# Optimization experiments

Measured on AMD Instinct MI355X. Metric: run time of the kernel, lower is better.

Reference implementation:

```python
import jax, jax.numpy as jnp
import numpy as np

N, E, F_IN, NCLS, H = 50000, 800000, 128, 10, 64


def setup_inputs() -> dict:
    key = jax.random.key(0)
    ks = jax.random.split(key, 24)
    p = lambda k, shp: (jax.random.normal(k, shp, dtype=jnp.float32) * 0.1)
    inp = {
        'x': jax.random.normal(ks[0], (N, F_IN), dtype=jnp.float32),
        'edge_index': jax.random.randint(ks[1], (2, E), 0, N, dtype=jnp.int64),
        'gcn1_W': p(ks[2], (F_IN, 128)), 'gcn1_b': p(ks[3], (128,)),
        'gcn2_W': p(ks[4], (128, 64)),  'gcn2_b': p(ks[5], (64,)),
        'gcn3_W': p(ks[6], (64, 32)),   'gcn3_b': p(ks[7], (32,)),
        'gat_W': p(ks[8], (32, 32)), 'gat_a_src': p(ks[9], (32,)),
        'gat_a_dst': p(ks[10], (32,)), 'gat_b': p(ks[11], (32,)),
        'lstm_Wih_f': p(ks[12], (4 * H, 32)), 'lstm_bih_f': p(ks[13], (4 * H,)), 'lstm_bhh_f': p(ks[14], (4 * H,)),
        'lstm_Wih_b': p(ks[15], (4 * H, 32)), 'lstm_bih_b': p(ks[16], (4 * H,)), 'lstm_bhh_b': p(ks[17], (4 * H,)),
        'bn_gamma': jnp.ones((2 * H,), jnp.float32), 'bn_beta': jnp.zeros((2 * H,), jnp.float32),
        'fc_W': p(ks[18], (NCLS, 2 * H)), 'fc_b': p(ks[19], (NCLS,)),
    }
    return inp


def _forward(x, edge_index, gcn1_W, gcn1_b, gcn2_W, gcn2_b, gcn3_W, gcn3_b,
             gat_W, gat_a_src, gat_a_dst, gat_b,
             lstm_Wih_f, lstm_bih_f, lstm_bhh_f, lstm_Wih_b, lstm_bih_b, lstm_bhh_b,
             bn_gamma, bn_beta, fc_W, fc_b):
    n = x.shape[0]
    loop = jnp.arange(n)
    row = jnp.concatenate([edge_index[0], loop])  # source nodes (+ self loops)
    col = jnp.concatenate([edge_index[1], loop])  # target nodes
    deg = jax.ops.segment_sum(jnp.ones_like(col, dtype=x.dtype), col, num_segments=n)
    dis = jax.lax.rsqrt(jnp.maximum(deg, 1e-12))  # deg >= 1 due to self loops
    norm = dis[row] * dis[col]

    def gcn(h, W, b):
        h = h @ W
        return jax.ops.segment_sum(h[row] * norm[:, None], col, num_segments=n) + b

    h = jax.nn.relu(gcn(x, gcn1_W, gcn1_b))
    h = jax.nn.relu(gcn(h, gcn2_W, gcn2_b))
    h = gcn(h, gcn3_W, gcn3_b)

    # GAT (1 head), self loops already in row/col, softmax over incoming edges per target
    g = h @ gat_W
    e = jax.nn.leaky_relu((g @ gat_a_src)[row] + (g @ gat_a_dst)[col], negative_slope=0.2)
    m = jax.ops.segment_max(e, col, num_segments=n)
    ee = jnp.exp(e - m[col])
    att = ee / jax.ops.segment_sum(ee, col, num_segments=n)[col]
    h = jax.ops.segment_sum(g[row] * att[:, None], col, num_segments=n) + gat_b
    h = jax.nn.relu(h)

    # bidirectional LSTM with seq_len=1, h0=c0=0 -> single cell step per direction
    def lstm_dir(xx, Wih, bih, bhh):
        gt = xx @ Wih.T + bih + bhh
        i, f, c, o = jnp.split(gt, 4, axis=-1)  # torch gate order i,f,g,o
        return jax.nn.sigmoid(o) * jnp.tanh(jax.nn.sigmoid(i) * jnp.tanh(c))

    r = jnp.concatenate([lstm_dir(h, lstm_Wih_f, lstm_bih_f, lstm_bhh_f),
                         lstm_dir(h, lstm_Wih_b, lstm_bih_b, lstm_bhh_b)], axis=-1)
    # eval mode: dropout = identity; BatchNorm1d with running_mean=0, running_var=1
    r = r * (bn_gamma / jnp.sqrt(jnp.float32(1.0 + 1e-5))) + bn_beta
    return r @ fc_W.T + fc_b


def reference(x, edge_index, gcn1_W, gcn1_b, gcn2_W, gcn2_b, gcn3_W, gcn3_b,
              gat_W, gat_a_src, gat_a_dst, gat_b,
              lstm_Wih_f, lstm_bih_f, lstm_bhh_f, lstm_Wih_b, lstm_bih_b, lstm_bhh_b,
              bn_gamma, bn_beta, fc_W, fc_b):
    return _forward(x, edge_index, gcn1_W, gcn1_b, gcn2_W, gcn2_b, gcn3_W, gcn3_b,
                    gat_W, gat_a_src, gat_a_dst, gat_b,
                    lstm_Wih_f, lstm_bih_f, lstm_bhh_f, lstm_Wih_b, lstm_bih_b, lstm_bhh_b,
                    bn_gamma, bn_beta, fc_W, fc_b)
```

## Files before the change

### kernel.cpp

```cpp
#include <hip/hip_runtime.h>
#include <hip/hip_bf16.h>
#include <math.h>

typedef __hip_bfloat16 bf16;
typedef __attribute__((ext_vector_type(8))) short short8v;
typedef __attribute__((ext_vector_type(4))) float f32x4;

#define NN 50000
#define EE 800000
#define EPB 4096
#define NBK 196
#define BCAP 6144

__device__ __forceinline__ float b2f(bf16 v) { return __bfloat162float(v); }
__device__ __forceinline__ float rcp_(float x) { return __builtin_amdgcn_rcpf(x); }
__device__ __forceinline__ float sigmoidf_(float x) { return rcp_(1.0f + __expf(-x)); }
__device__ __forceinline__ float tanhf_(float x) {
    float xx = fminf(fmaxf(x, -15.0f), 15.0f);
    float e = __expf(2.0f * xx);
    return (e - 1.0f) * rcp_(e + 1.0f);
}
__device__ __forceinline__ float leakyf_(float x) { return x > 0.0f ? x : 0.2f * x; }
__device__ __forceinline__ unsigned short f2bf(float f) {
    unsigned u = __float_as_uint(f);
    unsigned r = (u + 0x7FFFu + ((u >> 16) & 1u)) >> 16;
    return (unsigned short)r;
}
__device__ __forceinline__ unsigned pack2(float a, float b) {
    return (unsigned)f2bf(a) | ((unsigned)f2bf(b) << 16);
}
__device__ __forceinline__ float lo_(unsigned u) { return __uint_as_float(u << 16); }
__device__ __forceinline__ float hi_(unsigned u) { return __uint_as_float(u & 0xFFFF0000u); }

#define OFF_W1 0
#define OFF_B1 16384
#define OFF_W2 16512
#define OFF_B2 24704
#define OFF_W3 24768
#define OFF_B3 26816
#define OFF_GATW 26848
#define OFF_GAS 27872
#define OFF_GAD 27904
#define OFF_GAB 27936
#define OFF_WIHF 27968
#define OFF_BIHF 36160
#define OFF_BHHF 36416
#define OFF_WIHB 36672
#define OFF_BIHB 44864
#define OFF_BHHB 45120
#define OFF_GAMMA 45376
#define OFF_BETA 45504
#define OFF_FCW 45632
#define OFF_FCB 46912
#define WTOTAL 46922

#define AX_WT 0
#define AX_BT 12288
#define AX_GSC 12672
#define AX_GBE 12800
#define AX_TOTAL 12928

struct WSrc { const void* p[20]; };

__global__ void k_detect(const unsigned short* __restrict__ xraw,
                         const unsigned int* __restrict__ eraw, int* __restrict__ flags) {
    __shared__ int f32f, i64f;
    int t = threadIdx.x;
    if (t == 0) { f32f = 0; i64f = 1; }
    __syncthreads();
    for (int i = t; i < 4096; i += 256) {
        unsigned short u = xraw[i];
        int ex = (u >> 7) & 0xFF;
        if (ex >= 0xC0) atomicOr(&f32f, 1);
        if (eraw[2 * i + 1] != 0u) atomicAnd(&i64f, 0);
    }
    __syncthreads();
    if (t == 0) { flags[0] = f32f; flags[1] = i64f; }
}

__global__ void k_cvt_w(WSrc srcs, float* __restrict__ dst, const int* __restrict__ flags,
                        int total) {
    constexpr int WOFF[21] = {OFF_W1,   OFF_B1,   OFF_W2,   OFF_B2,   OFF_W3,   OFF_B3,
                              OFF_GATW, OFF_GAS,  OFF_GAD,  OFF_GAB,  OFF_WIHF, OFF_BIHF,
                              OFF_BHHF, OFF_WIHB, OFF_BIHB, OFF_BHHB, OFF_GAMMA, OFF_BETA,
                              OFF_FCW,  OFF_FCB,  WTOTAL};
    int i = blockIdx.x * 256 + threadIdx.x;
    if (i >= total) return;
    int tn = 0;
#pragma unroll
    for (int j = 1; j < 20; ++j)
        if (i >= WOFF[j]) tn = j;
    int local = i - WOFF[tn];
    if (flags[0]) dst[i] = ((const float*)srcs.p[tn])[local];
    else dst[i] = b2f(((const bf16*)srcs.p[tn])[local]);
}

__global__ void k_prep(const float* __restrict__ wp, float* __restrict__ aux) {
    int dir = blockIdx.x;
    int t = threadIdx.x;
    const float* W = wp + (dir ? OFF_WIHB : OFF_WIHF);
    const float* bi = wp + (dir ? OFF_BIHB : OFF_BIHF);
    const float* bh = wp + (dir ? OFF_BHHB : OFF_BHHF);
    int col = t;
    int j = col / 3, gate = col - 3 * j;
    int srcrow = j + (gate == 1 ? 128 : (gate == 2 ? 192 : 0));
    const float* src = W + (size_t)srcrow * 32;
    for (int k = 0; k < 32; ++k) aux[AX_WT + dir * 6144 + k * 192 + col] = src[k];
    aux[AX_BT + dir * 192 + col] = bi[srcrow] + bh[srcrow];
    if (t < 64) {
        int jj = dir * 64 + t;
        aux[AX_GSC + jj] = wp[OFF_GAMMA + jj] * rsqrtf(1.0f + 1e-5f);
        aux[AX_GBE + jj] = wp[OFF_BETA + jj];
    }
}

__global__ void k_prep_w1(const float* __restrict__ wp, unsigned short* __restrict__ wsplit) {
    int t = blockIdx.x * 256 + threadIdx.x;
    if (t >= 16384) return;
    int k = t >> 7, col = t & 127;
    float w = wp[OFF_W1 + k * 128 + col];
    unsigned short hi = f2bf(w);
    float hif = __uint_as_float((unsigned)hi << 16);
    unsigned short lo = f2bf(w - hif);
    int kt = k >> 5, kk = k & 31;
    wsplit[((size_t)(kt * 2 + 0) * 128 + col) * 32 + kk] = hi;
    wsplit[((size_t)(kt * 2 + 1) * 128 + col) * 32 + kk] = lo;
}

__global__ __launch_bounds__(256) void k_hist(const void* __restrict__ eraw,
                                              unsigned* __restrict__ gh,
                                              const int* __restrict__ flags) {
    __shared__ int h[256];
    int t = threadIdx.x, b = blockIdx.x;
    h[t] = 0;
    __syncthreads();
    int e0 = b * EPB;
    bool i64 = flags[1] != 0;
    for (int i = t; i < EPB; i += 256) {
        int e = e0 + i;
        if (e < EE) {
            int d = i64 ? (int)((const long long*)eraw)[EE + e] : ((const int*)eraw)[EE + e];
            d = min(max(d, 0), NN - 1);
            atomicAdd(&h[d >> 8], 1);
        }
    }
    __syncthreads();
    gh[b * 256 + t] = (unsigned)h[t];
}

__global__ __launch_bounds__(256) void k_bscan(const unsigned* __restrict__ gh,
                                               unsigned* __restrict__ gh2,
                                               int* __restrict__ bb, int* __restrict__ rptr) {
    __shared__ int s[256];
    int t = threadIdx.x;
    unsigned run = 0;
    for (int blk = 0; blk < NBK; ++blk) {
        unsigned v = gh[blk * 256 + t];
        gh2[blk * 256 + t] = run;
        run += v;
    }
    s[t] = (int)run;
    __syncthreads();
    for (int o = 1; o < 256; o <<= 1) {
        int x = (t >= o) ? s[t - o] : 0;
        __syncthreads();
        s[t] += x;
        __syncthreads();
    }
    bb[t] = s[t] - (int)run;
    if (t == 0) rptr[NN] = EE;
}

__global__ __launch_bounds__(256) void k_scatter(const void* __restrict__ eraw,
                                                 const unsigned* __restrict__ gh2,
                                                 const int* __restrict__ bb,
                                                 int2* __restrict__ ebkt,
                                                 const int* __restrict__ flags) {
    __shared__ unsigned cur[256];
    int t = threadIdx.x, b = blockIdx.x;
    cur[t] = gh2[b * 256 + t] + (unsigned)bb[t];
    __syncthreads();
    int e0 = b * EPB;
    bool i64 = flags[1] != 0;
    for (int i = t; i < EPB; i += 256) {
        int e = e0 + i;
        if (e < EE) {
            int sn, d;
            if (i64) {
                sn = (int)((const long long*)eraw)[e];
                d = (int)((const long long*)eraw)[EE + e];
            } else {
                sn = ((const int*)eraw)[e];
                d = ((const int*)eraw)[EE + e];
            }
            sn = min(max(sn, 0), NN - 1);
            d = min(max(d, 0), NN - 1);
            unsigned pos = atomicAdd(&cur[d >> 8], 1u);
            if (pos < (unsigned)EE) ebkt[pos] = make_int2(sn, d);
        }
    }
}

__global__ __launch_bounds__(256) void k_bucket_csr(const int2* __restrict__ ebkt,
                                                    const int* __restrict__ bb,
                                                    int* __restrict__ rptr,
                                                    float* __restrict__ dis,
                                                    int* __restrict__ csr_src) {
    __shared__ int hist[256];
    __shared__ int excl[256];
    __shared__ int cur[256];
    __shared__ int sorted[BCAP];
    int t = threadIdx.x, b = blockIdx.x;
    int s0 = bb[b], s1 = bb[b + 1];
    int len = min(s1 - s0, BCAP);
    hist[t] = 0;
    __syncthreads();
    for (int i = t; i < len; i += 256) atomicAdd(&hist[ebkt[s0 + i].y & 255], 1);
    __syncthreads();
    int v = hist[t];
    excl[t] = v;
    __syncthreads();
    for (int o = 1; o < 256; o <<= 1) {
        int x = (t >= o) ? excl[t - o] : 0;
        __syncthreads();
        excl[t] += x;
        __syncthreads();
    }
    int loc = excl[t] - v;
    int node = b * 256 + t;
    if (node < NN) {
        rptr[node] = s0 + loc;
        dis[node] = rsqrtf((float)(v + 1));
    }
    cur[t] = loc;
    __syncthreads();
    for (int i = t; i < len; i += 256) {
        int2 p = ebkt[s0 + i];
        int pos = atomicAdd(&cur[p.y & 255], 1);
        if (pos < BCAP) sorted[pos] = p.x;
    }
    __syncthreads();
    for (int i = t; i < len; i += 256) csr_src[s0 + i] = sorted[i];
}

template <int MODE>
__global__ __launch_bounds__(256) void k_gcn1_mfma(const void* __restrict__ A,
                                                   const unsigned short* __restrict__ wsplit,
                                                   unsigned* __restrict__ C, int n,
                                                   const int* __restrict__ flags,
                                                   const float* __restrict__ dis) {
    if (flags[0] != MODE) return;
    __shared__ unsigned short Ah[64 * 136];
    __shared__ unsigned short Al[MODE ? 64 * 136 : 4];
    __shared__ unsigned short Wh[128 * 40];
    __shared__ unsigned short Wl[128 * 40];
    int t = threadIdx.x;
    int l = t & 63, w = t >> 6;
    int base = blockIdx.x * 64;
    if constexpr (MODE == 0) {
#pragma unroll
        for (int p = 0; p < 4; ++p) {
            int c = p * 256 + t;
            int nd = c >> 4, ko = (c & 15) * 8;
            int node = min(base + nd, n - 1);
            uint4 v = *(const uint4*)((const unsigned short*)A + (size_t)node * 128 + ko);
            *(uint4*)(Ah + nd * 136 + ko) = v;
        }
    } else {
#pragma unroll
        for (int p = 0; p < 8; ++p) {
            int c = p * 256 + t;
            int nd = c >> 5, ko = (c & 31) * 4;
            int node = min(base + nd, n - 1);
            float4 v = *(const float4*)((const float*)A + (size_t)node * 128 + ko);
            ushort4 hi, lo;
            hi.x = f2bf(v.x); lo.x = f2bf(v.x - __uint_as_float((unsigned)hi.x << 16));
            hi.y = f2bf(v.y); lo.y = f2bf(v.y - __uint_as_float((unsigned)hi.y << 16));
            hi.z = f2bf(v.z); lo.z = f2bf(v.z - __uint_as_float((unsigned)hi.z << 16));
            hi.w = f2bf(v.w); lo.w = f2bf(v.w - __uint_as_float((unsigned)hi.w << 16));
            *(ushort4*)(Ah + nd * 136 + ko) = hi;
            *(ushort4*)(Al + nd * 136 + ko) = lo;
        }
    }
    int wr = (w >> 1) * 32, wc = (w & 1) * 64;
    int lrow = l & 15, lk = (l >> 4) * 8;
    f32x4 acc[2][4];
#pragma unroll
    for (int rb = 0; rb < 2; ++rb)
#pragma unroll
        for (int cb = 0; cb < 4; ++cb) acc[rb][cb] = (f32x4){0.f, 0.f, 0.f, 0.f};
    for (int kt = 0; kt < 4; ++kt) {
        __syncthreads();
#pragma unroll
        for (int p = 0; p < 2; ++p) {
            int c = p * 256 + t;
            int col = c >> 2, ko = (c & 3) * 8;
            *(uint4*)(Wh + col * 40 + ko) =
                *(const uint4*)(wsplit + ((size_t)(kt * 2 + 0) * 128 + col) * 32 + ko);
            *(uint4*)(Wl + col * 40 + ko) =
                *(const uint4*)(wsplit + ((size_t)(kt * 2 + 1) * 128 + col) * 32 + ko);
        }
        __syncthreads();
        short8v ah0 = *(const short8v*)(Ah + (wr + lrow) * 136 + kt * 32 + lk);
        short8v ah1 = *(const short8v*)(Ah + (wr + 16 + lrow) * 136 + kt * 32 + lk);
        short8v al0, al1;
        if constexpr (MODE == 1) {
            al0 = *(const short8v*)(Al + (wr + lrow) * 136 + kt * 32 + lk);
            al1 = *(const short8v*)(Al + (wr + 16 + lrow) * 136 + kt * 32 + lk);
        }
#pragma unroll
        for (int cb = 0; cb < 4; ++cb) {
            int col = wc + cb * 16 + lrow;
            short8v bh = *(const short8v*)(Wh + col * 40 + lk);
            short8v bl = *(const short8v*)(Wl + col * 40 + lk);
            acc[0][cb] = __builtin_amdgcn_mfma_f32_16x16x32_bf16(ah0, bh, acc[0][cb], 0, 0, 0);
            acc[0][cb] = __builtin_amdgcn_mfma_f32_16x16x32_bf16(ah0, bl, acc[0][cb], 0, 0, 0);
            acc[1][cb] = __builtin_amdgcn_mfma_f32_16x16x32_bf16(ah1, bh, acc[1][cb], 0, 0, 0);
            acc[1][cb] = __builtin_amdgcn_mfma_f32_16x16x32_bf16(ah1, bl, acc[1][cb], 0, 0, 0);
            if constexpr (MODE == 1) {
                acc[0][cb] = __builtin_amdgcn_mfma_f32_16x16x32_bf16(al0, bh, acc[0][cb], 0, 0, 0);
                acc[1][cb] = __builtin_amdgcn_mfma_f32_16x16x32_bf16(al1, bh, acc[1][cb], 0, 0, 0);
            }
        }
    }
#pragma unroll
    for (int rb = 0; rb < 2; ++rb) {
#pragma unroll
        for (int reg = 0; reg < 4; ++reg) {
            int row = wr + rb * 16 + (l >> 4) * 4 + reg;
            int node = base + row;
            if (node < n) {
                float sc = dis[node];
                unsigned short* cr = (unsigned short*)C + (size_t)node * 128;
#pragma unroll
                for (int cb = 0; cb < 4; ++cb) {
                    int col = wc + cb * 16 + lrow;
                    cr[col] = f2bf(acc[rb][cb][reg] * sc);
                }
            }
        }
    }
}

template <int KIN, int KOUT, int MODE, bool SCALE>
__global__ __launch_bounds__(256) void k_tile_mm(const void* __restrict__ A,
                                                 const float* __restrict__ W,
                                                 unsigned* __restrict__ C, int n,
                                                 const int* __restrict__ flags, int want,
                                                 const float* __restrict__ dis) {
    if (want >= 0 && flags[0] != want) return;
    constexpr int BK = 32;
    constexpr int AST = BK + 4;
    constexpr int CPT = KOUT / 16;
    __shared__ float As[64 * AST];
    __shared__ float Ws[BK * KOUT];
    int t = threadIdx.x;
    int jc = t & 15;
    int ng = t >> 4;
    int base = blockIdx.x * 64;
    float acc[4][CPT];
#pragma unroll
    for (int i = 0; i < 4; ++i)
#pragma unroll
        for (int c = 0; c < CPT; ++c) acc[i][c] = 0.f;
    int snode = t >> 2;
    int gnode = min(base + snode, n - 1);
    int koff = (t & 3) * 8;
    for (int k0 = 0; k0 < KIN; k0 += BK) {
        {
            const float4* src = (const float4*)(W + k0 * KOUT);
            float4* dst = (float4*)Ws;
#pragma unroll
            for (int p = 0; p < BK * KOUT / 1024; ++p) dst[t + p * 256] = src[t + p * 256];
        }
        if (MODE == 0) {
            const unsigned* xr = (const unsigned*)A + (size_t)gnode * (KIN / 2) + (k0 + koff) / 2;
            unsigned u0 = xr[0], u1 = xr[1], u2 = xr[2], u3 = xr[3];
            float* d = As + snode * AST + koff;
            d[0] = lo_(u0); d[1] = hi_(u0);
            d[2] = lo_(u1); d[3] = hi_(u1);
            d[4] = lo_(u2); d[5] = hi_(u2);
            d[6] = lo_(u3); d[7] = hi_(u3);
        } else {
            const float4* ar = (const float4*)((const float*)A + (size_t)gnode * KIN + k0 + koff);
            float4 v0 = ar[0], v1 = ar[1];
            float4* d = (float4*)(As + snode * AST + koff);
            d[0] = v0;
            d[1] = v1;
        }
        __syncthreads();
#pragma unroll 8
        for (int k = 0; k < BK; ++k) {
            float w[CPT];
            const float* wr = Ws + k * KOUT + jc * CPT;
            if constexpr (CPT >= 4) {
#pragma unroll
                for (int c = 0; c < CPT; c += 4) {
                    float4 wv = *(const float4*)(wr + c);
                    w[c] = wv.x; w[c + 1] = wv.y; w[c + 2] = wv.z; w[c + 3] = wv.w;
                }
            } else {
                float2 wv = *(const float2*)wr;
                w[0] = wv.x; w[1] = wv.y;
            }
            float a0 = As[(ng * 4 + 0) * AST + k];
            float a1 = As[(ng * 4 + 1) * AST + k];
            float a2 = As[(ng * 4 + 2) * AST + k];
            float a3 = As[(ng * 4 + 3) * AST + k];
#pragma unroll
            for (int c = 0; c < CPT; ++c) {
                acc[0][c] += a0 * w[c];
                acc[1][c] += a1 * w[c];
                acc[2][c] += a2 * w[c];
                acc[3][c] += a3 * w[c];
            }
        }
        __syncthreads();
    }
#pragma unroll
    for (int i = 0; i < 4; ++i) {
        int node = base + ng * 4 + i;
        if (node < n) {
            float sc = SCALE ? dis[node] : 1.0f;
            unsigned* cr = C + (size_t)node * (KOUT / 2) + jc * (CPT / 2);
#pragma unroll
            for (int c = 0; c < CPT; c += 2)
                cr[c / 2] = pack2(acc[i][c] * sc, acc[i][c + 1] * sc);
        }
    }
}

template <bool RELU>
__global__ void k_agg128(const unsigned* __restrict__ t, const int* __restrict__ rptr,
                         const int* __restrict__ csr_src, const float* __restrict__ dis,
                         const float* __restrict__ bias, float* __restrict__ out, int n) {
    int wave = (blockIdx.x * blockDim.x + threadIdx.x) >> 6;
    int lane = threadIdx.x & 63;
    if (wave >= n) return;
    int dst = wave;
    float dd = dis[dst];
    float ax, ay;
    {
        unsigned u = t[(size_t)dst * 64 + lane];
        ax = lo_(u);
        ay = hi_(u);
    }
    int s = __builtin_amdgcn_readfirstlane(max(0, min(rptr[dst], EE)));
    int e = __builtin_amdgcn_readfirstlane(max(s, min(rptr[dst + 1], EE)));
    int j = s;
    for (; j + 8 <= e; j += 8) {
        int i0 = csr_src[j], i1 = csr_src[j + 1], i2 = csr_src[j + 2], i3 = csr_src[j + 3];
        int i4 = csr_src[j + 4], i5 = csr_src[j + 5], i6 = csr_src[j + 6], i7 = csr_src[j + 7];
        unsigned u0 = t[(size_t)i0 * 64 + lane], u1 = t[(size_t)i1 * 64 + lane];
        unsigned u2 = t[(size_t)i2 * 64 + lane], u3 = t[(size_t)i3 * 64 + lane];
        unsigned u4 = t[(size_t)i4 * 64 + lane], u5 = t[(size_t)i5 * 64 + lane];
        unsigned u6 = t[(size_t)i6 * 64 + lane], u7 = t[(size_t)i7 * 64 + lane];
        ax += (lo_(u0) + lo_(u1)) + (lo_(u2) + lo_(u3)) + (lo_(u4) + lo_(u5)) + (lo_(u6) + lo_(u7));
        ay += (hi_(u0) + hi_(u1)) + (hi_(u2) + hi_(u3)) + (hi_(u4) + hi_(u5)) + (hi_(u6) + hi_(u7));
    }
    for (; j + 4 <= e; j += 4) {
        int i0 = csr_src[j], i1 = csr_src[j + 1], i2 = csr_src[j + 2], i3 = csr_src[j + 3];
        unsigned u0 = t[(size_t)i0 * 64 + lane], u1 = t[(size_t)i1 * 64 + lane];
        unsigned u2 = t[(size_t)i2 * 64 + lane], u3 = t[(size_t)i3 * 64 + lane];
        ax += (lo_(u0) + lo_(u1)) + (lo_(u2) + lo_(u3));
        ay += (hi_(u0) + hi_(u1)) + (hi_(u2) + hi_(u3));
    }
    for (; j < e; ++j) {
        unsigned u0 = t[(size_t)csr_src[j] * 64 + lane];
        ax += lo_(u0);
        ay += hi_(u0);
    }
    float2 bv = *(const float2*)(bias + 2 * lane);
    float vx = ax * dd + bv.x;
    float vy = ay * dd + bv.y;
    if (RELU) { vx = fmaxf(vx, 0.f); vy = fmaxf(vy, 0.f); }
    *(float2*)(out + (size_t)dst * 128 + 2 * lane) = make_float2(vx, vy);
}

template <bool RELU>
__global__ void k_agg64(const unsigned* __restrict__ t, const int* __restrict__ rptr,
                        const int* __restrict__ csr_src, const float* __restrict__ dis,
                        const float* __restrict__ bias, float* __restrict__ out, int n) {
    int wave = (blockIdx.x * blockDim.x + threadIdx.x) >> 6;
    int lane = threadIdx.x & 63;
    if (wave >= n) return;
    int dst = wave;
    int half = lane >> 5, l32 = lane & 31;
    float dd = dis[dst];
    float ax = 0.f, ay = 0.f;
    if (!half) {
        unsigned u = t[(size_t)dst * 32 + l32];
        ax = lo_(u);
        ay = hi_(u);
    }
    int s = max(0, min(rptr[dst], EE));
    int e = max(s, min(rptr[dst + 1], EE));
    int cnt = e - s;
    int pairs = cnt >> 1;
    int p = 0;
    for (; p + 4 <= pairs; p += 4) {
        int jb = s + 2 * p + half;
        int i0 = csr_src[jb], i1 = csr_src[jb + 2], i2 = csr_src[jb + 4], i3 = csr_src[jb + 6];
        unsigned u0 = t[(size_t)i0 * 32 + l32], u1 = t[(size_t)i1 * 32 + l32];
        unsigned u2 = t[(size_t)i2 * 32 + l32], u3 = t[(size_t)i3 * 32 + l32];
        ax += (lo_(u0) + lo_(u1)) + (lo_(u2) + lo_(u3));
        ay += (hi_(u0) + hi_(u1)) + (hi_(u2) + hi_(u3));
    }
    for (; p < pairs; ++p) {
        int i0 = csr_src[s + 2 * p + half];
        unsigned u0 = t[(size_t)i0 * 32 + l32];
        ax += lo_(u0);
        ay += hi_(u0);
    }
    if ((cnt & 1) && !half) {
        unsigned u0 = t[(size_t)csr_src[e - 1] * 32 + l32];
        ax += lo_(u0);
        ay += hi_(u0);
    }
    ax += __shfl_down(ax, 32);
    ay += __shfl_down(ay, 32);
    if (!half) {
        float2 bv = *(const float2*)(bias + 2 * l32);
        float vx = ax * dd + bv.x;
        float vy = ay * dd + bv.y;
        if (RELU) { vx = fmaxf(vx, 0.f); vy = fmaxf(vy, 0.f); }
        *(float2*)(out + (size_t)dst * 64 + 2 * l32) = make_float2(vx, vy);
    }
}

template <bool RELU>
__global__ void k_agg32(const unsigned* __restrict__ t, const int* __restrict__ rptr,
                        const int* __restrict__ csr_src, const float* __restrict__ dis,
                        const float* __restrict__ bias, float* __restrict__ out, int n) {
    int wave = (blockIdx.x * blockDim.x + threadIdx.x) >> 6;
    int lane = threadIdx.x & 63;
    if (wave >= n) return;
    int dst = wave;
    int q = lane >> 4, l16 = lane & 15;
    float dd = dis[dst];
    float ax = 0.f, ay = 0.f;
    if (q == 0) {
        unsigned u = t[(size_t)dst * 16 + l16];
        ax = lo_(u);
        ay = hi_(u);
    }
    int s = max(0, min(rptr[dst], EE));
    int e = max(s, min(rptr[dst + 1], EE));
    int cnt = e - s;
    int quads = cnt >> 2;
    int p = 0;
    for (; p + 4 <= quads; p += 4) {
        int jb = s + 4 * p + q;
        int i0 = csr_src[jb], i1 = csr_src[jb + 4], i2 = csr_src[jb + 8], i3 = csr_src[jb + 12];
        unsigned u0 = t[(size_t)i0 * 16 + l16], u1 = t[(size_t)i1 * 16 + l16];
        unsigned u2 = t[(size_t)i2 * 16 + l16], u3 = t[(size_t)i3 * 16 + l16];
        ax += (lo_(u0) + lo_(u1)) + (lo_(u2) + lo_(u3));
        ay += (hi_(u0) + hi_(u1)) + (hi_(u2) + hi_(u3));
    }
    for (; p < quads; ++p) {
        int i0 = csr_src[s + 4 * p + q];
        unsigned u0 = t[(size_t)i0 * 16 + l16];
        ax += lo_(u0);
        ay += hi_(u0);
    }
    int rem = cnt - 4 * quads;
    if (q < rem) {
        unsigned u0 = t[(size_t)csr_src[s + 4 * quads + q] * 16 + l16];
        ax += lo_(u0);
        ay += hi_(u0);
    }
    ax += __shfl_down(ax, 32);
    ay += __shfl_down(ay, 32);
    ax += __shfl_down(ax, 16);
    ay += __shfl_down(ay, 16);
    if (q == 0) {
        float2 bv = *(const float2*)(bias + 2 * l16);
        float vx = ax * dd + bv.x;
        float vy = ay * dd + bv.y;
        if (RELU) { vx = fmaxf(vx, 0.f); vy = fmaxf(vy, 0.f); }
        *(float2*)(out + (size_t)dst * 32 + 2 * l16) = make_float2(vx, vy);
    }
}

__global__ void k_gat_vec(const unsigned* __restrict__ g, const float* __restrict__ a_src,
                          const float* __restrict__ a_dst, float* __restrict__ asrc,
                          float* __restrict__ adst, int n) {
    int i = blockIdx.x * 256 + threadIdx.x;
    if (i >= n) return;
    float s = 0.0f, d = 0.0f;
    const unsigned* gr = g + (size_t)i * 16;
#pragma unroll
    for (int k = 0; k < 16; ++k) {
        unsigned u = gr[k];
        float v0 = lo_(u), v1 = hi_(u);
        s += v0 * a_src[2 * k] + v1 * a_src[2 * k + 1];
        d += v0 * a_dst[2 * k] + v1 * a_dst[2 * k + 1];
    }
    asrc[i] = s;
    adst[i] = d;
}

__global__ void k_gat_agg(const unsigned* __restrict__ g, const int* __restrict__ rptr,
                          const int* __restrict__ csr_src, const float* __restrict__ asrc,
                          const float* __restrict__ adst, const float* __restrict__ gat_b,
                          float* __restrict__ out, int n) {
    int wave = (blockIdx.x * blockDim.x + threadIdx.x) >> 6;
    int lane = threadIdx.x & 63;
    if (wave >= n) return;
    int dst = wave;
    int q = lane >> 4, l16 = lane & 15;
    float ad = adst[dst];
    int s = max(0, min(rptr[dst], EE));
    int e = max(s, min(rptr[dst + 1], EE));
    float ax = 0.f, ay = 0.f, denom = 0.f;
    if (q == 0) {
        float w0 = __expf(fminf(leakyf_(asrc[dst] + ad), 80.f));
        unsigned u = g[(size_t)dst * 16 + l16];
        ax = lo_(u) * w0;
        ay = hi_(u) * w0;
        denom = w0;
    }
    int cnt = e - s;
    int quads = cnt >> 2;
    int p = 0;
    for (; p + 4 <= quads; p += 4) {
        int jb = s + 4 * p + q;
        int i0 = csr_src[jb], i1 = csr_src[jb + 4], i2 = csr_src[jb + 8], i3 = csr_src[jb + 12];
        float a0 = asrc[i0], a1 = asrc[i1], a2 = asrc[i2], a3 = asrc[i3];
        unsigned u0 = g[(size_t)i0 * 16 + l16], u1 = g[(size_t)i1 * 16 + l16];
        unsigned u2 = g[(size_t)i2 * 16 + l16], u3 = g[(size_t)i3 * 16 + l16];
        float w0 = __expf(fminf(leakyf_(a0 + ad), 80.f));
        float w1 = __expf(fminf(leakyf_(a1 + ad), 80.f));
        float w2 = __expf(fminf(leakyf_(a2 + ad), 80.f));
        float w3 = __expf(fminf(leakyf_(a3 + ad), 80.f));
        denom += (w0 + w1) + (w2 + w3);
        ax += lo_(u0) * w0 + lo_(u1) * w1 + lo_(u2) * w2 + lo_(u3) * w3;
        ay += hi_(u0) * w0 + hi_(u1) * w1 + hi_(u2) * w2 + hi_(u3) * w3;
    }
    for (; p < quads; ++p) {
        int i0 = csr_src[s + 4 * p + q];
        float wgt = __expf(fminf(leakyf_(asrc[i0] + ad), 80.f));
        unsigned u0 = g[(size_t)i0 * 16 + l16];
        denom += wgt;
        ax += lo_(u0) * wgt;
        ay += hi_(u0) * wgt;
    }
    int rem = cnt - 4 * quads;
    if (q < rem) {
        int i0 = csr_src[s + 4 * quads + q];
        float wgt = __expf(fminf(leakyf_(asrc[i0] + ad), 80.f));
        unsigned u0 = g[(size_t)i0 * 16 + l16];
        denom += wgt;
        ax += lo_(u0) * wgt;
        ay += hi_(u0) * wgt;
    }
    ax += __shfl_down(ax, 32);
    ay += __shfl_down(ay, 32);
    denom += __shfl_down(denom, 32);
    ax += __shfl_down(ax, 16);
    ay += __shfl_down(ay, 16);
    denom += __shfl_down(denom, 16);
    if (q == 0) {
        float r = rcp_(denom);
        float vx = fmaxf(ax * r + gat_b[2 * l16], 0.f);
        float vy = fmaxf(ay * r + gat_b[2 * l16 + 1], 0.f);
        *(float2*)(out + (size_t)dst * 32 + 2 * l16) = make_float2(vx, vy);
    }
}

__global__ __launch_bounds__(256) void k_gates(const float* __restrict__ h,
                                               const float* __restrict__ aux,
                                               float* __restrict__ rbuf, int n) {
    constexpr int AST = 36;
    __shared__ float As[64 * AST];
    __shared__ float Ws[32 * 192];
    int t = threadIdx.x;
    int dir = blockIdx.y;
    int jc = t & 15;
    int ng = t >> 4;
    int base = blockIdx.x * 64;
    {
        const float4* src = (const float4*)(aux + AX_WT + dir * 6144);
        float4* dst = (float4*)Ws;
#pragma unroll
        for (int p = 0; p < 6; ++p) dst[t + p * 256] = src[t + p * 256];
    }
    {
        int snode = t >> 2;
        int gnode = min(base + snode, n - 1);
        int koff = (t & 3) * 8;
        const float4* ar = (const float4*)(h + (size_t)gnode * 32 + koff);
        float4* d = (float4*)(As + snode * AST + koff);
        d[0] = ar[0];
        d[1] = ar[1];
    }
    float acc[4][12];
    {
        const float4* bt = (const float4*)(aux + AX_BT + dir * 192 + jc * 12);
        float4 b0 = bt[0], b1 = bt[1], b2 = bt[2];
        float b12[12] = {b0.x, b0.y, b0.z, b0.w, b1.x, b1.y, b1.z, b1.w,
                         b2.x, b2.y, b2.z, b2.w};
#pragma unroll
        for (int i = 0; i < 4; ++i)
#pragma unroll
            for (int c = 0; c < 12; ++c) acc[i][c] = b12[c];
    }
    __syncthreads();
#pragma unroll 8
    for (int k = 0; k < 32; ++k) {
        float w[12];
        const float* wr = Ws + k * 192 + jc * 12;
#pragma unroll
        for (int c = 0; c < 12; c += 4) {
            float4 wv = *(const float4*)(wr + c);
            w[c] = wv.x; w[c + 1] = wv.y; w[c + 2] = wv.z; w[c + 3] = wv.w;
        }
        float a0 = As[(ng * 4 + 0) * AST + k];
        float a1 = As[(ng * 4 + 1) * AST + k];
        float a2 = As[(ng * 4 + 2) * AST + k];
        float a3 = As[(ng * 4 + 3) * AST + k];
#pragma unroll
        for (int c = 0; c < 12; ++c) {
            acc[0][c] += a0 * w[c];
            acc[1][c] += a1 * w[c];
            acc[2][c] += a2 * w[c];
            acc[3][c] += a3 * w[c];
        }
    }
    float4 gscv = *(const float4*)(aux + AX_GSC + dir * 64 + jc * 4);
    float4 gbev = *(const float4*)(aux + AX_GBE + dir * 64 + jc * 4);
#pragma unroll
    for (int i = 0; i < 4; ++i) {
        int node = base + ng * 4 + i;
        if (node < n) {
            float v0 = sigmoidf_(acc[i][2]) * tanhf_(sigmoidf_(acc[i][0]) * tanhf_(acc[i][1]));
            float v1 = sigmoidf_(acc[i][5]) * tanhf_(sigmoidf_(acc[i][3]) * tanhf_(acc[i][4]));
            float v2 = sigmoidf_(acc[i][8]) * tanhf_(sigmoidf_(acc[i][6]) * tanhf_(acc[i][7]));
            float v3 = sigmoidf_(acc[i][11]) * tanhf_(sigmoidf_(acc[i][9]) * tanhf_(acc[i][10]));
            float4 rv;
            rv.x = v0 * gscv.x + gbev.x;
            rv.y = v1 * gscv.y + gbev.y;
            rv.z = v2 * gscv.z + gbev.z;
            rv.w = v3 * gscv.w + gbev.w;
            *(float4*)(rbuf + (size_t)node * 128 + dir * 64 + jc * 4) = rv;
        }
    }
}

__global__ __launch_bounds__(256) void k_fc(const float* __restrict__ rbuf,
                                            const float* __restrict__ wp,
                                            void* __restrict__ out,
                                            const int* __restrict__ flags, int n) {
    __shared__ float rs[64 * 129];
    __shared__ float ps[4 * 640];
    int t = threadIdx.x;
    int base = blockIdx.x * 64;
    for (int i = t; i < 2048; i += 256) {
        int nd = i >> 5, k4 = i & 31;
        int node = min(base + nd, n - 1);
        float4 v = ((const float4*)rbuf)[(size_t)node * 32 + k4];
        float* d = rs + nd * 129 + k4 * 4;
        d[0] = v.x; d[1] = v.y; d[2] = v.z; d[3] = v.w;
    }
    __syncthreads();
    {
        int nd = t & 63, quarter = t >> 6;
        const float* fcw = wp + OFF_FCW;
        int jbase = quarter * 32;
        float p10[10];
#pragma unroll
        for (int c = 0; c < 10; ++c) p10[c] = 0.f;
#pragma unroll 4
        for (int k = 0; k < 32; ++k) {
            float r = rs[nd * 129 + jbase + k];
#pragma unroll
            for (int c = 0; c < 10; ++c) p10[c] += r * fcw[c * 128 + jbase + k];
        }
#pragma unroll
        for (int c = 0; c < 10; ++c) ps[quarter * 640 + nd * 10 + c] = p10[c];
    }
    __syncthreads();
    bool f32o = flags[0] != 0;
    for (int idx = t; idx < 640; idx += 256) {
        int gnode = base + idx / 10;
        if (gnode < n) {
            int c = idx % 10;
            float v = wp[OFF_FCB + c] + ps[idx] + ps[640 + idx] + ps[1280 + idx] + ps[1920 + idx];
            if (f32o) ((float*)out)[(size_t)base * 10 + idx] = v;
            else ((unsigned short*)out)[(size_t)base * 10 + idx] = f2bf(v);
        }
    }
}

extern "C" void kernel_launch(void* const* d_in, const int* in_sizes, int n_in,
                              void* d_out, int out_size, void* d_ws, size_t ws_size,
                              hipStream_t stream) {
    const int N = NN;

    char* w = (char*)d_ws;
    auto alloc = [&](size_t bytes) {
        void* p = (void*)w;
        w += (bytes + 255) & ~(size_t)255;
        return p;
    };
    int* flags = (int*)alloc(256);
    float* wpool = (float*)alloc((size_t)WTOTAL * 4);
    float* aux = (float*)alloc((size_t)AX_TOTAL * 4);
    unsigned short* wsplit = (unsigned short*)alloc(65536);
    float* dis = (float*)alloc((size_t)N * 4);
    int* rptr = (int*)alloc((size_t)(N + 1) * 4);
    int* csr_src = (int*)alloc((size_t)EE * 4);
    unsigned* gh = (unsigned*)alloc((size_t)NBK * 256 * 4);
    unsigned* gh2 = (unsigned*)alloc((size_t)NBK * 256 * 4);
    int* bb = (int*)alloc(1024);
    int2* ebkt = (int2*)alloc((size_t)EE * 8);
    float* asrc = (float*)alloc((size_t)N * 4);
    float* adst = (float*)alloc((size_t)N * 4);
    unsigned* bufT = (unsigned*)alloc((size_t)N * 64 * 4);
    float* bufH = (float*)alloc((size_t)N * 128 * 4);
    float* rbuf = (float*)alloc((size_t)N * 128 * 4);

    WSrc ws_srcs;
    for (int i = 0; i < 20; ++i) ws_srcs.p[i] = d_in[2 + i];

    const int NB = (N + 255) / 256;
    const int AGG = (N + 3) / 4;
    const int TMB = (N + 63) / 64;
    const int WB = (WTOTAL + 255) / 256;

    k_detect<<<1, 256, 0, stream>>>((const unsigned short*)d_in[0],
                                    (const unsigned int*)d_in[1], flags);
    k_cvt_w<<<WB, 256, 0, stream>>>(ws_srcs, wpool, flags, WTOTAL);
    k_prep<<<2, 192, 0, stream>>>(wpool, aux);
    k_prep_w1<<<64, 256, 0, stream>>>(wpool, wsplit);
    k_hist<<<NBK, 256, 0, stream>>>(d_in[1], gh, flags);
    k_bscan<<<1, 256, 0, stream>>>(gh, gh2, bb, rptr);
    k_scatter<<<NBK, 256, 0, stream>>>(d_in[1], gh2, bb, ebkt, flags);
    k_bucket_csr<<<NBK, 256, 0, stream>>>(ebkt, bb, rptr, dis, csr_src);

    k_gcn1_mfma<0><<<TMB, 256, 0, stream>>>(d_in[0], wsplit, bufT, N, flags, dis);
    k_gcn1_mfma<1><<<TMB, 256, 0, stream>>>(d_in[0], wsplit, bufT, N, flags, dis);
    k_agg128<true><<<AGG, 256, 0, stream>>>(bufT, rptr, csr_src, dis, wpool + OFF_B1, bufH, N);
    k_tile_mm<128, 64, 1, true><<<TMB, 256, 0, stream>>>(bufH, wpool + OFF_W2, bufT, N, flags, -1, dis);
    k_agg64<true><<<AGG, 256, 0, stream>>>(bufT, rptr, csr_src, dis, wpool + OFF_B2, bufH, N);
    k_tile_mm<64, 32, 1, true><<<TMB, 256, 0, stream>>>(bufH, wpool + OFF_W3, bufT, N, flags, -1, dis);
    k_agg32<false><<<AGG, 256, 0, stream>>>(bufT, rptr, csr_src, dis, wpool + OFF_B3, bufH, N);
    k_tile_mm<32, 32, 1, false><<<TMB, 256, 0, stream>>>(bufH, wpool + OFF_GATW, bufT, N, flags, -1, dis);
    k_gat_vec<<<NB, 256, 0, stream>>>(bufT, wpool + OFF_GAS, wpool + OFF_GAD, asrc, adst, N);
    k_gat_agg<<<AGG, 256, 0, stream>>>(bufT, rptr, csr_src, asrc, adst, wpool + OFF_GAB, bufH, N);
    k_gates<<<dim3(TMB, 2), 256, 0, stream>>>(bufH, aux, rbuf, N);
    k_fc<<<TMB, 256, 0, stream>>>(rbuf, wpool, d_out, flags, N);
}
```

Before: 362.9 us.

## Move dense GCN, GAT and LSTM gate matmuls to split-bf16 MFMA kernels

```diff
diff --git a/kernel.cpp b/kernel.cpp
--- a/kernel.cpp
+++ b/kernel.cpp
@@ -31,6 +31,12 @@
 }
 __device__ __forceinline__ float lo_(unsigned u) { return __uint_as_float(u << 16); }
 __device__ __forceinline__ float hi_(unsigned u) { return __uint_as_float(u & 0xFFFF0000u); }
+__device__ __forceinline__ void split4(float4 v, ushort4& hi, ushort4& lo) {
+    hi.x = f2bf(v.x); lo.x = f2bf(v.x - __uint_as_float((unsigned)hi.x << 16));
+    hi.y = f2bf(v.y); lo.y = f2bf(v.y - __uint_as_float((unsigned)hi.y << 16));
+    hi.z = f2bf(v.z); lo.z = f2bf(v.z - __uint_as_float((unsigned)hi.z << 16));
+    hi.w = f2bf(v.w); lo.w = f2bf(v.w - __uint_as_float((unsigned)hi.w << 16));
+}
 
 #define OFF_W1 0
 #define OFF_B1 16384
@@ -54,12 +60,6 @@
 #define OFF_FCB 46912
 #define WTOTAL 46922
 
-#define AX_WT 0
-#define AX_BT 12288
-#define AX_GSC 12672
-#define AX_GBE 12800
-#define AX_TOTAL 12928
-
 struct WSrc { const void* p[20]; };
 
 __global__ void k_detect(const unsigned short* __restrict__ xraw,
@@ -93,25 +93,6 @@
     int local = i - WOFF[tn];
     if (flags[0]) dst[i] = ((const float*)srcs.p[tn])[local];
     else dst[i] = b2f(((const bf16*)srcs.p[tn])[local]);
-}
-
-__global__ void k_prep(const float* __restrict__ wp, float* __restrict__ aux) {
-    int dir = blockIdx.x;
-    int t = threadIdx.x;
-    const float* W = wp + (dir ? OFF_WIHB : OFF_WIHF);
-    const float* bi = wp + (dir ? OFF_BIHB : OFF_BIHF);
-    const float* bh = wp + (dir ? OFF_BHHB : OFF_BHHF);
-    int col = t;
-    int j = col / 3, gate = col - 3 * j;
-    int srcrow = j + (gate == 1 ? 128 : (gate == 2 ? 192 : 0));
-    const float* src = W + (size_t)srcrow * 32;
-    for (int k = 0; k < 32; ++k) aux[AX_WT + dir * 6144 + k * 192 + col] = src[k];
-    aux[AX_BT + dir * 192 + col] = bi[srcrow] + bh[srcrow];
-    if (t < 64) {
-        int jj = dir * 64 + t;
-        aux[AX_GSC + jj] = wp[OFF_GAMMA + jj] * rsqrtf(1.0f + 1e-5f);
-        aux[AX_GBE + jj] = wp[OFF_BETA + jj];
-    }
 }
 
 __global__ void k_prep_w1(const float* __restrict__ wp, unsigned short* __restrict__ wsplit) {
@@ -125,6 +106,34 @@
     int kt = k >> 5, kk = k & 31;
     wsplit[((size_t)(kt * 2 + 0) * 128 + col) * 32 + kk] = hi;
     wsplit[((size_t)(kt * 2 + 1) * 128 + col) * 32 + kk] = lo;
+}
+
+template <int KIN, int KOUT>
+__global__ void k_prep_ws(const float* __restrict__ src, unsigned short* __restrict__ dst) {
+    int i = blockIdx.x * 256 + threadIdx.x;
+    if (i >= KIN * KOUT) return;
+    int k = i / KOUT, col = i % KOUT;
+    float w = src[(size_t)k * KOUT + col];
+    unsigned short hi = f2bf(w);
+    unsigned short lo = f2bf(w - __uint_as_float((unsigned)hi << 16));
+    int kt = k >> 5, kk = k & 31;
+    dst[((size_t)(kt * 2 + 0) * KOUT + col) * 32 + kk] = hi;
+    dst[((size_t)(kt * 2 + 1) * KOUT + col) * 32 + kk] = lo;
+}
+
+__global__ void k_prep_wg(const float* __restrict__ wp, unsigned short* __restrict__ wsg) {
+    int t = blockIdx.x * 256 + threadIdx.x;
+    if (t >= 12288) return;
+    int dir = t / 6144, r2 = t % 6144;
+    int row = r2 >> 5, k = r2 & 31;
+    int gate = row >> 6, j = row & 63;
+    int srcrow = j + (gate == 1 ? 128 : (gate == 2 ? 192 : 0));
+    const float* W = wp + (dir ? OFF_WIHB : OFF_WIHF);
+    float w = W[(size_t)srcrow * 32 + k];
+    unsigned short hi = f2bf(w);
+    unsigned short lo = f2bf(w - __uint_as_float((unsigned)hi << 16));
+    wsg[((size_t)(dir * 2 + 0) * 192 + row) * 32 + k] = hi;
+    wsg[((size_t)(dir * 2 + 1) * 192 + row) * 32 + k] = lo;
 }
 
 __global__ __launch_bounds__(256) void k_hist(const void* __restrict__ eraw,
@@ -274,10 +283,7 @@
             int node = min(base + nd, n - 1);
             float4 v = *(const float4*)((const float*)A + (size_t)node * 128 + ko);
             ushort4 hi, lo;
-            hi.x = f2bf(v.x); lo.x = f2bf(v.x - __uint_as_float((unsigned)hi.x << 16));
-            hi.y = f2bf(v.y); lo.y = f2bf(v.y - __uint_as_float((unsigned)hi.y << 16));
-            hi.z = f2bf(v.z); lo.z = f2bf(v.z - __uint_as_float((unsigned)hi.z << 16));
-            hi.w = f2bf(v.w); lo.w = f2bf(v.w - __uint_as_float((unsigned)hi.w << 16));
+            split4(v, hi, lo);
             *(ushort4*)(Ah + nd * 136 + ko) = hi;
             *(ushort4*)(Al + nd * 136 + ko) = lo;
         }
@@ -342,90 +348,81 @@
     }
 }
 
-template <int KIN, int KOUT, int MODE, bool SCALE>
-__global__ __launch_bounds__(256) void k_tile_mm(const void* __restrict__ A,
-                                                 const float* __restrict__ W,
-                                                 unsigned* __restrict__ C, int n,
-                                                 const int* __restrict__ flags, int want,
+template <int KIN, int KOUT, bool SCALE>
+__global__ __launch_bounds__(256) void k_mm_mfma(const float* __restrict__ A,
+                                                 const unsigned short* __restrict__ wsplit,
+                                                 unsigned short* __restrict__ C, int n,
                                                  const float* __restrict__ dis) {
-    if (want >= 0 && flags[0] != want) return;
-    constexpr int BK = 32;
-    constexpr int AST = BK + 4;
-    constexpr int CPT = KOUT / 16;
-    __shared__ float As[64 * AST];
-    __shared__ float Ws[BK * KOUT];
+    constexpr int AST = KIN + 8;
+    constexpr int KT = KIN / 32;
+    constexpr int CB = KOUT / 32;
+    __shared__ unsigned short Ah[64 * AST];
+    __shared__ unsigned short Al[64 * AST];
+    __shared__ unsigned short Wh[KOUT * 40];
+    __shared__ unsigned short Wl[KOUT * 40];
     int t = threadIdx.x;
-    int jc = t & 15;
-    int ng = t >> 4;
+    int l = t & 63, w = t >> 6;
     int base = blockIdx.x * 64;
-    float acc[4][CPT];
-#pragma unroll
-    for (int i = 0; i < 4; ++i)
-#pragma unroll
-        for (int c = 0; c < CPT; ++c) acc[i][c] = 0.f;
-    int snode = t >> 2;
-    int gnode = min(base + snode, n - 1);
-    int koff = (t & 3) * 8;
-    for (int k0 = 0; k0 < KIN; k0 += BK) {
-        {
-            const float4* src = (const float4*)(W + k0 * KOUT);
-            float4* dst = (float4*)Ws;
-#pragma unroll
-            for (int p = 0; p < BK * KOUT / 1024; ++p) dst[t + p * 256] = src[t + p * 256];
-        }
-        if (MODE == 0) {
-            const unsigned* xr = (const unsigned*)A + (size_t)gnode * (KIN / 2) + (k0 + koff) / 2;
-            unsigned u0 = xr[0], u1 = xr[1], u2 = xr[2], u3 = xr[3];
-            float* d = As + snode * AST + koff;
-            d[0] = lo_(u0); d[1] = hi_(u0);
-            d[2] = lo_(u1); d[3] = hi_(u1);
-            d[4] = lo_(u2); d[5] = hi_(u2);
-            d[6] = lo_(u3); d[7] = hi_(u3);
-        } else {
-            const float4* ar = (const float4*)((const float*)A + (size_t)gnode * KIN + k0 + koff);
-            float4 v0 = ar[0], v1 = ar[1];
-            float4* d = (float4*)(As + snode * AST + koff);
-            d[0] = v0;
-            d[1] = v1;
-        }
+#pragma unroll
+    for (int p = 0; p < KIN / 16; ++p) {
+        int c = p * 256 + t;
+        int nd = c / (KIN / 4), ko = (c % (KIN / 4)) * 4;
+        int node = min(base + nd, n - 1);
+        float4 v = *(const float4*)(A + (size_t)node * KIN + ko);
+        ushort4 hi, lo;
+        split4(v, hi, lo);
+        *(ushort4*)(Ah + nd * AST + ko) = hi;
+        *(ushort4*)(Al + nd * AST + ko) = lo;
+    }
+    int wr = (w >> 1) * 32, wc = (w & 1) * (KOUT / 2);
+    int lrow = l & 15, lk = (l >> 4) * 8;
+    f32x4 acc[2][CB];
+#pragma unroll
+    for (int rb = 0; rb < 2; ++rb)
+#pragma unroll
+        for (int cb = 0; cb < CB; ++cb) acc[rb][cb] = (f32x4){0.f, 0.f, 0.f, 0.f};
+    for (int kt = 0; kt < KT; ++kt) {
         __syncthreads();
-#pragma unroll 8
-        for (int k = 0; k < BK; ++k) {
-            float w[CPT];
-            const float* wr = Ws + k * KOUT + jc * CPT;
-            if constexpr (CPT >= 4) {
-#pragma unroll
-                for (int c = 0; c < CPT; c += 4) {
-                    float4 wv = *(const float4*)(wr + c);
-                    w[c] = wv.x; w[c + 1] = wv.y; w[c + 2] = wv.z; w[c + 3] = wv.w;
+        for (int c = t; c < KOUT * 4; c += 256) {
+            int col = c >> 2, ko = (c & 3) * 8;
+            *(uint4*)(Wh + col * 40 + ko) =
+                *(const uint4*)(wsplit + ((size_t)(kt * 2 + 0) * KOUT + col) * 32 + ko);
+            *(uint4*)(Wl + col * 40 + ko) =
+                *(const uint4*)(wsplit + ((size_t)(kt * 2 + 1) * KOUT + col) * 32 + ko);
+        }
+        __syncthreads();
+        short8v ah0 = *(const short8v*)(Ah + (wr + lrow) * AST + kt * 32 + lk);
+        short8v ah1 = *(const short8v*)(Ah + (wr + 16 + lrow) * AST + kt * 32 + lk);
+        short8v al0 = *(const short8v*)(Al + (wr + lrow) * AST + kt * 32 + lk);
+        short8v al1 = *(const short8v*)(Al + (wr + 16 + lrow) * AST + kt * 32 + lk);
+#pragma unroll
+        for (int cb = 0; cb < CB; ++cb) {
+            int col = wc + cb * 16 + lrow;
+            short8v bh = *(const short8v*)(Wh + col * 40 + lk);
+            short8v bl = *(const short8v*)(Wl + col * 40 + lk);
+            acc[0][cb] = __builtin_amdgcn_mfma_f32_16x16x32_bf16(ah0, bh, acc[0][cb], 0, 0, 0);
+            acc[0][cb] = __builtin_amdgcn_mfma_f32_16x16x32_bf16(ah0, bl, acc[0][cb], 0, 0, 0);
+            acc[0][cb] = __builtin_amdgcn_mfma_f32_16x16x32_bf16(al0, bh, acc[0][cb], 0, 0, 0);
+            acc[1][cb] = __builtin_amdgcn_mfma_f32_16x16x32_bf16(ah1, bh, acc[1][cb], 0, 0, 0);
+            acc[1][cb] = __builtin_amdgcn_mfma_f32_16x16x32_bf16(ah1, bl, acc[1][cb], 0, 0, 0);
+            acc[1][cb] = __builtin_amdgcn_mfma_f32_16x16x32_bf16(al1, bh, acc[1][cb], 0, 0, 0);
+        }
+    }
+#pragma unroll
+    for (int rb = 0; rb < 2; ++rb) {
+#pragma unroll
+        for (int reg = 0; reg < 4; ++reg) {
+            int row = wr + rb * 16 + (l >> 4) * 4 + reg;
+            int node = base + row;
+            if (node < n) {
+                float sc = SCALE ? dis[node] : 1.0f;
+                unsigned short* cr = C + (size_t)node * KOUT;
+#pragma unroll
+                for (int cb = 0; cb < CB; ++cb) {
+                    int col = wc + cb * 16 + lrow;
+                    cr[col] = f2bf(acc[rb][cb][reg] * sc);
                 }
-            } else {
-                float2 wv = *(const float2*)wr;
-                w[0] = wv.x; w[1] = wv.y;
             }
-            float a0 = As[(ng * 4 + 0) * AST + k];
-            float a1 = As[(ng * 4 + 1) * AST + k];
-            float a2 = As[(ng * 4 + 2) * AST + k];
-            float a3 = As[(ng * 4 + 3) * AST + k];
-#pragma unroll
-            for (int c = 0; c < CPT; ++c) {
-                acc[0][c] += a0 * w[c];
-                acc[1][c] += a1 * w[c];
-                acc[2][c] += a2 * w[c];
-                acc[3][c] += a3 * w[c];
-            }
-        }
-        __syncthreads();
-    }
-#pragma unroll
-    for (int i = 0; i < 4; ++i) {
-        int node = base + ng * 4 + i;
-        if (node < n) {
-            float sc = SCALE ? dis[node] : 1.0f;
-            unsigned* cr = C + (size_t)node * (KOUT / 2) + jc * (CPT / 2);
-#pragma unroll
-            for (int c = 0; c < CPT; c += 2)
-                cr[c / 2] = pack2(acc[i][c] * sc, acc[i][c + 1] * sc);
         }
     }
 }
@@ -668,86 +665,83 @@
     }
 }
 
-__global__ __launch_bounds__(256) void k_gates(const float* __restrict__ h,
-                                               const float* __restrict__ aux,
-                                               float* __restrict__ rbuf, int n) {
-    constexpr int AST = 36;
-    __shared__ float As[64 * AST];
-    __shared__ float Ws[32 * 192];
+__global__ __launch_bounds__(256) void k_gates_mfma(const float* __restrict__ h,
+                                                    const unsigned short* __restrict__ wsg,
+                                                    const float* __restrict__ wp,
+                                                    float* __restrict__ rbufT, int n) {
+    __shared__ unsigned short Ah[64 * 40];
+    __shared__ unsigned short Al[64 * 40];
+    __shared__ unsigned short Wh[192 * 40];
+    __shared__ unsigned short Wl[192 * 40];
+    __shared__ float bI[64], bG[64], bO[64], gs[64], gb[64];
     int t = threadIdx.x;
     int dir = blockIdx.y;
-    int jc = t & 15;
-    int ng = t >> 4;
+    int l = t & 63, w = t >> 6;
     int base = blockIdx.x * 64;
+#pragma unroll
+    for (int p = 0; p < 2; ++p) {
+        int c = p * 256 + t;
+        int nd = c >> 3, ko = (c & 7) * 4;
+        int node = min(base + nd, n - 1);
+        float4 v = *(const float4*)(h + (size_t)node * 32 + ko);
+        ushort4 hi, lo;
+        split4(v, hi, lo);
+        *(ushort4*)(Ah + nd * 40 + ko) = hi;
+        *(ushort4*)(Al + nd * 40 + ko) = lo;
+    }
     {
-        const float4* src = (const float4*)(aux + AX_WT + dir * 6144);
-        float4* dst = (float4*)Ws;
-#pragma unroll
-        for (int p = 0; p < 6; ++p) dst[t + p * 256] = src[t + p * 256];
-    }
-    {
-        int snode = t >> 2;
-        int gnode = min(base + snode, n - 1);
-        int koff = (t & 3) * 8;
-        const float4* ar = (const float4*)(h + (size_t)gnode * 32 + koff);
-        float4* d = (float4*)(As + snode * AST + koff);
-        d[0] = ar[0];
-        d[1] = ar[1];
-    }
-    float acc[4][12];
-    {
-        const float4* bt = (const float4*)(aux + AX_BT + dir * 192 + jc * 12);
-        float4 b0 = bt[0], b1 = bt[1], b2 = bt[2];
-        float b12[12] = {b0.x, b0.y, b0.z, b0.w, b1.x, b1.y, b1.z, b1.w,
-                         b2.x, b2.y, b2.z, b2.w};
-#pragma unroll
-        for (int i = 0; i < 4; ++i)
-#pragma unroll
-            for (int c = 0; c < 12; ++c) acc[i][c] = b12[c];
-    }
-    __syncthreads();
-#pragma unroll 8
-    for (int k = 0; k < 32; ++k) {
-        float w[12];
-        const float* wr = Ws + k * 192 + jc * 12;
-#pragma unroll
-        for (int c = 0; c < 12; c += 4) {
-            float4 wv = *(const float4*)(wr + c);
-            w[c] = wv.x; w[c + 1] = wv.y; w[c + 2] = wv.z; w[c + 3] = wv.w;
-        }
-        float a0 = As[(ng * 4 + 0) * AST + k];
-        float a1 = As[(ng * 4 + 1) * AST + k];
-        float a2 = As[(ng * 4 + 2) * AST + k];
-        float a3 = As[(ng * 4 + 3) * AST + k];
-#pragma unroll
-        for (int c = 0; c < 12; ++c) {
-            acc[0][c] += a0 * w[c];
-            acc[1][c] += a1 * w[c];
-            acc[2][c] += a2 * w[c];
-            acc[3][c] += a3 * w[c];
-        }
-    }
-    float4 gscv = *(const float4*)(aux + AX_GSC + dir * 64 + jc * 4);
-    float4 gbev = *(const float4*)(aux + AX_GBE + dir * 64 + jc * 4);
-#pragma unroll
-    for (int i = 0; i < 4; ++i) {
-        int node = base + ng * 4 + i;
-        if (node < n) {
-            float v0 = sigmoidf_(acc[i][2]) * tanhf_(sigmoidf_(acc[i][0]) * tanhf_(acc[i][1]));
-            float v1 = sigmoidf_(acc[i][5]) * tanhf_(sigmoidf_(acc[i][3]) * tanhf_(acc[i][4]));
-            float v2 = sigmoidf_(acc[i][8]) * tanhf_(sigmoidf_(acc[i][6]) * tanhf_(acc[i][7]));
-            float v3 = sigmoidf_(acc[i][11]) * tanhf_(sigmoidf_(acc[i][9]) * tanhf_(acc[i][10]));
-            float4 rv;
-            rv.x = v0 * gscv.x + gbev.x;
-            rv.y = v1 * gscv.y + gbev.y;
-            rv.z = v2 * gscv.z + gbev.z;
-            rv.w = v3 * gscv.w + gbev.w;
-            *(float4*)(rbuf + (size_t)node * 128 + dir * 64 + jc * 4) = rv;
-        }
-    }
-}
-
-__global__ __launch_bounds__(256) void k_fc(const float* __restrict__ rbuf,
+        const unsigned short* sh = wsg + (size_t)(dir * 2 + 0) * 192 * 32;
+        const unsigned short* sl = wsg + (size_t)(dir * 2 + 1) * 192 * 32;
+#pragma unroll
+        for (int p = 0; p < 3; ++p) {
+            int c = p * 256 + t;
+            int row = c >> 2, ko = (c & 3) * 8;
+            *(uint4*)(Wh + row * 40 + ko) = *(const uint4*)(sh + (size_t)row * 32 + ko);
+            *(uint4*)(Wl + row * 40 + ko) = *(const uint4*)(sl + (size_t)row * 32 + ko);
+        }
+    }
+    if (t < 64) {
+        const float* bi_ = wp + (dir ? OFF_BIHB : OFF_BIHF);
+        const float* bh_ = wp + (dir ? OFF_BHHB : OFF_BHHF);
+        bI[t] = bi_[t] + bh_[t];
+        bG[t] = bi_[128 + t] + bh_[128 + t];
+        bO[t] = bi_[192 + t] + bh_[192 + t];
+        gs[t] = wp[OFF_GAMMA + dir * 64 + t] * rsqrtf(1.0f + 1e-5f);
+        gb[t] = wp[OFF_BETA + dir * 64 + t];
+    }
+    __syncthreads();
+    int lrow = l & 15, lk = (l >> 4) * 8;
+    short8v hh = *(const short8v*)(Ah + (w * 16 + lrow) * 40 + lk);
+    short8v hl = *(const short8v*)(Al + (w * 16 + lrow) * 40 + lk);
+    f32x4 acc[12];
+#pragma unroll
+    for (int m = 0; m < 12; ++m) acc[m] = (f32x4){0.f, 0.f, 0.f, 0.f};
+#pragma unroll
+    for (int m = 0; m < 12; ++m) {
+        short8v wh = *(const short8v*)(Wh + (m * 16 + lrow) * 40 + lk);
+        short8v wl = *(const short8v*)(Wl + (m * 16 + lrow) * 40 + lk);
+        acc[m] = __builtin_amdgcn_mfma_f32_16x16x32_bf16(wh, hh, acc[m], 0, 0, 0);
+        acc[m] = __builtin_amdgcn_mfma_f32_16x16x32_bf16(wl, hh, acc[m], 0, 0, 0);
+        acc[m] = __builtin_amdgcn_mfma_f32_16x16x32_bf16(wh, hl, acc[m], 0, 0, 0);
+    }
+    int node = base + w * 16 + lrow;
+    if (node < n) {
+#pragma unroll
+        for (int m = 0; m < 4; ++m) {
+#pragma unroll
+            for (int reg = 0; reg < 4; ++reg) {
+                int j = 16 * m + (l >> 4) * 4 + reg;
+                float iv = acc[m][reg] + bI[j];
+                float gv = acc[m + 4][reg] + bG[j];
+                float ov = acc[m + 8][reg] + bO[j];
+                float v = sigmoidf_(ov) * tanhf_(sigmoidf_(iv) * tanhf_(gv));
+                rbufT[(size_t)(dir * 64 + j) * NN + node] = v * gs[j] + gb[j];
+            }
+        }
+    }
+}
+
+__global__ __launch_bounds__(256) void k_fc(const float* __restrict__ rbufT,
                                             const float* __restrict__ wp,
                                             void* __restrict__ out,
                                             const int* __restrict__ flags, int n) {
@@ -755,12 +749,10 @@
     __shared__ float ps[4 * 640];
     int t = threadIdx.x;
     int base = blockIdx.x * 64;
-    for (int i = t; i < 2048; i += 256) {
-        int nd = i >> 5, k4 = i & 31;
+    for (int i = t; i < 8192; i += 256) {
+        int jj = i >> 6, nd = i & 63;
         int node = min(base + nd, n - 1);
-        float4 v = ((const float4*)rbuf)[(size_t)node * 32 + k4];
-        float* d = rs + nd * 129 + k4 * 4;
-        d[0] = v.x; d[1] = v.y; d[2] = v.z; d[3] = v.w;
+        rs[nd * 129 + jj] = rbufT[(size_t)jj * NN + node];
     }
     __syncthreads();
     {
@@ -805,8 +797,11 @@
     };
     int* flags = (int*)alloc(256);
     float* wpool = (float*)alloc((size_t)WTOTAL * 4);
-    float* aux = (float*)alloc((size_t)AX_TOTAL * 4);
     unsigned short* wsplit = (unsigned short*)alloc(65536);
+    unsigned short* ws2 = (unsigned short*)alloc(32768);
+    unsigned short* ws3 = (unsigned short*)alloc(8192);
+    unsigned short* wsgat = (unsigned short*)alloc(4096);
+    unsigned short* wsg = (unsigned short*)alloc(49152);
     float* dis = (float*)alloc((size_t)N * 4);
     int* rptr = (int*)alloc((size_t)(N + 1) * 4);
     int* csr_src = (int*)alloc((size_t)EE * 4);
@@ -818,7 +813,7 @@
     float* adst = (float*)alloc((size_t)N * 4);
     unsigned* bufT = (unsigned*)alloc((size_t)N * 64 * 4);
     float* bufH = (float*)alloc((size_t)N * 128 * 4);
-    float* rbuf = (float*)alloc((size_t)N * 128 * 4);
+    float* rbufT = (float*)alloc((size_t)N * 128 * 4);
 
     WSrc ws_srcs;
     for (int i = 0; i < 20; ++i) ws_srcs.p[i] = d_in[2 + i];
@@ -831,8 +826,11 @@
     k_detect<<<1, 256, 0, stream>>>((const unsigned short*)d_in[0],
                                     (const unsigned int*)d_in[1], flags);
     k_cvt_w<<<WB, 256, 0, stream>>>(ws_srcs, wpool, flags, WTOTAL);
-    k_prep<<<2, 192, 0, stream>>>(wpool, aux);
     k_prep_w1<<<64, 256, 0, stream>>>(wpool, wsplit);
+    k_prep_ws<128, 64><<<32, 256, 0, stream>>>(wpool + OFF_W2, ws2);
+    k_prep_ws<64, 32><<<8, 256, 0, stream>>>(wpool + OFF_W3, ws3);
+    k_prep_ws<32, 32><<<4, 256, 0, stream>>>(wpool + OFF_GATW, wsgat);
+    k_prep_wg<<<48, 256, 0, stream>>>(wpool, wsg);
     k_hist<<<NBK, 256, 0, stream>>>(d_in[1], gh, flags);
     k_bscan<<<1, 256, 0, stream>>>(gh, gh2, bb, rptr);
     k_scatter<<<NBK, 256, 0, stream>>>(d_in[1], gh2, bb, ebkt, flags);
@@ -841,13 +839,13 @@
     k_gcn1_mfma<0><<<TMB, 256, 0, stream>>>(d_in[0], wsplit, bufT, N, flags, dis);
     k_gcn1_mfma<1><<<TMB, 256, 0, stream>>>(d_in[0], wsplit, bufT, N, flags, dis);
     k_agg128<true><<<AGG, 256, 0, stream>>>(bufT, rptr, csr_src, dis, wpool + OFF_B1, bufH, N);
-    k_tile_mm<128, 64, 1, true><<<TMB, 256, 0, stream>>>(bufH, wpool + OFF_W2, bufT, N, flags, -1, dis);
+    k_mm_mfma<128, 64, true><<<TMB, 256, 0, stream>>>(bufH, ws2, (unsigned short*)bufT, N, dis);
     k_agg64<true><<<AGG, 256, 0, stream>>>(bufT, rptr, csr_src, dis, wpool + OFF_B2, bufH, N);
-    k_tile_mm<64, 32, 1, true><<<TMB, 256, 0, stream>>>(bufH, wpool + OFF_W3, bufT, N, flags, -1, dis);
+    k_mm_mfma<64, 32, true><<<TMB, 256, 0, stream>>>(bufH, ws3, (unsigned short*)bufT, N, dis);
     k_agg32<false><<<AGG, 256, 0, stream>>>(bufT, rptr, csr_src, dis, wpool + OFF_B3, bufH, N);
-    k_tile_mm<32, 32, 1, false><<<TMB, 256, 0, stream>>>(bufH, wpool + OFF_GATW, bufT, N, flags, -1, dis);
+    k_mm_mfma<32, 32, false><<<TMB, 256, 0, stream>>>(bufH, wsgat, (unsigned short*)bufT, N, dis);
     k_gat_vec<<<NB, 256, 0, stream>>>(bufT, wpool + OFF_GAS, wpool + OFF_GAD, asrc, adst, N);
     k_gat_agg<<<AGG, 256, 0, stream>>>(bufT, rptr, csr_src, asrc, adst, wpool + OFF_GAB, bufH, N);
-    k_gates<<<dim3(TMB, 2), 256, 0, stream>>>(bufH, aux, rbuf, N);
-    k_fc<<<TMB, 256, 0, stream>>>(rbuf, wpool, d_out, flags, N);
-}
+    k_gates_mfma<<<dim3(TMB, 2), 256, 0, stream>>>(bufH, wsg, wpool, rbufT, N);
+    k_fc<<<TMB, 256, 0, stream>>>(rbufT, wpool, d_out, flags, N);
+}
```

Result: faster. 353.6 us (-2.5%).
